# Kernel tuning notes

Hardware: AMD Instinct MI355X
Metric: run time of the kernel (lower is better)

The kernel has to match this reference:

```python
import jax, jax.numpy as jnp
import numpy as np

LL = 1 << 20            # Fastfood padded size (power of 2 >= DD)
DD = 1024 * 768         # out_features * in_features
OUT, IN = 1024, 768


def fwht(v):
    """Unnormalized fast Walsh-Hadamard transform over a length-2^k vector."""
    n = v.shape[0]
    h = 1
    while h < n:
        v = v.reshape(-1, 2, h)
        v = jnp.concatenate([v[:, 0] + v[:, 1], v[:, 0] - v[:, 1]], axis=-1)
        h *= 2
    return v.reshape(n)


def setup_inputs() -> dict:
    key = jax.random.key(0)
    ks = jax.random.split(key, 7)
    x = jax.random.normal(ks[0], (8, 2048, IN), dtype=jnp.float32)
    theta = jax.random.normal(ks[1], (2048,), dtype=jnp.float32)
    W_0 = jax.random.normal(ks[2], (OUT, IN), dtype=jnp.float32) * 0.02
    b = jax.random.normal(ks[3], (OUT,), dtype=jnp.float32) * 0.02
    # Rademacher +/-1 diagonal
    BB = (jax.random.bernoulli(ks[4], 0.5, (LL,)).astype(jnp.float32) * 2.0 - 1.0)
    GG = jax.random.normal(ks[5], (LL,), dtype=jnp.float32)
    Pi = jax.random.permutation(ks[6], LL).astype(jnp.int64)
    return {"x": x, "theta": theta, "W_0": W_0, "b": b, "BB": BB, "GG": GG, "Pi": Pi}


def reference(x, theta, W_0, b, BB, GG, Pi):
    # pad intrinsic parameter to LL (theta.numel() < LL branch)
    theta_pad = jnp.zeros((LL,), dtype=theta.dtype).at[: theta.shape[0]].set(theta)
    # Fastfood: H B theta -> permute -> G diag -> H
    v = fwht(BB * theta_pad)
    v = v[Pi] * GG
    v = fwht(v)
    divisor = jnp.sqrt(LL * jnp.sum(GG * GG))
    update_vec = v[:DD] / (divisor * np.sqrt(float(DD) / LL))
    W_eff = W_0 + update_vec.reshape(OUT, IN)
    return jnp.einsum("bsi,oi->bso", x, W_eff) + b
```

## Files before the change

kernel.cpp:

```cpp
#include <hip/hip_runtime.h>
#include <hip/hip_bf16.h>


#define LL (1 << 20)
#define DD (1024 * 768)
#define OUTF 1024
#define INF 768
#define MROWS 16384

typedef __attribute__((ext_vector_type(8))) short s16x8;
typedef __attribute__((ext_vector_type(4))) float f32x4;

__device__ __forceinline__ unsigned short f2bf(float f) {
    union { float f; unsigned u; } v; v.f = f;
    unsigned r = v.u + 0x7FFF + ((v.u >> 16) & 1);
    return (unsigned short)(r >> 16);
}

__global__ void k3_gather_fwht_lo(const int* __restrict__ Pi, const float* __restrict__ GG,
                                  const float* __restrict__ BB, const float* __restrict__ theta,
                                  float* __restrict__ T, float* __restrict__ partial) {
    __shared__ float s[1024];
    __shared__ float r01s[2048];
    __shared__ float ws4[4];
    const int tid = threadIdx.x;
    const int row = blockIdx.x;
    const int4   pv = ((const int4*)Pi)[row * 256 + tid];
    const float4 gv = ((const float4*)GG)[row * 256 + tid];
    for (int j = tid; j < 2048; j += 256) r01s[j] = BB[j] * theta[j];
    for (int h = 1; h < 1024; h <<= 1) {
        __syncthreads();
        for (int w = tid; w < 1024; w += 256) {
            int rr = w >> 9;
            int b  = w & 511;
            int bh = b & (h - 1);
            int i  = ((b - bh) << 1) + bh + rr * 1024;
            float a = r01s[i], c = r01s[i + h];
            r01s[i] = a + c; r01s[i + h] = a - c;
        }
    }
    float g2 = gv.x * gv.x + gv.y * gv.y + gv.z * gv.z + gv.w * gv.w;
    #pragma unroll
    for (int o = 32; o > 0; o >>= 1) g2 += __shfl_down(g2, o, 64);
    if ((tid & 63) == 0) ws4[tid >> 6] = g2;
    __syncthreads();
    {
        int p; float g, v;
        p = pv.x; g = gv.x;
        v = (r01s[p & 1023] + (((p >> 10) & 1) ? -1.0f : 1.0f) * r01s[1024 + (p & 1023)]) * g;
        s[tid * 4 + 0] = v;
        p = pv.y; g = gv.y;
        v = (r01s[p & 1023] + (((p >> 10) & 1) ? -1.0f : 1.0f) * r01s[1024 + (p & 1023)]) * g;
        s[tid * 4 + 1] = v;
        p = pv.z; g = gv.z;
        v = (r01s[p & 1023] + (((p >> 10) & 1) ? -1.0f : 1.0f) * r01s[1024 + (p & 1023)]) * g;
        s[tid * 4 + 2] = v;
        p = pv.w; g = gv.w;
        v = (r01s[p & 1023] + (((p >> 10) & 1) ? -1.0f : 1.0f) * r01s[1024 + (p & 1023)]) * g;
        s[tid * 4 + 3] = v;
    }
    for (int h = 1; h < 1024; h <<= 1) {
        __syncthreads();
        for (int w = tid; w < 512; w += 256) {
            int bh = w & (h - 1);
            int i  = ((w - bh) << 1) + bh;
            float a = s[i], c = s[i + h];
            s[i] = a + c; s[i + h] = a - c;
        }
    }
    __syncthreads();
    float4 v;
    v.x = s[tid * 4 + 0]; v.y = s[tid * 4 + 1]; v.z = s[tid * 4 + 2]; v.w = s[tid * 4 + 3];
    ((float4*)T)[row * 256 + tid] = v;
    if (tid == 0) partial[row] = ws4[0] + ws4[1] + ws4[2] + ws4[3];
}

__global__ void k4_fwht_hi(float* __restrict__ T, const float* __restrict__ partial,
                           float* __restrict__ S) {
    __shared__ float s[8 * 1025];
    __shared__ float rw[4];
    const int tid = threadIdx.x;
    if (blockIdx.x == 0) {
        float p = partial[tid] + partial[tid + 256] + partial[tid + 512] + partial[tid + 768];
        #pragma unroll
        for (int o = 32; o > 0; o >>= 1) p += __shfl_down(p, o, 64);
        if ((tid & 63) == 0) rw[tid >> 6] = p;
        __syncthreads();
        if (tid == 0) *S = rw[0] + rw[1] + rw[2] + rw[3];
    }
    const int lo0 = blockIdx.x * 8;
    float4* T4 = (float4*)T;
    const int hio = tid >> 1;
    const int q   = tid & 1;
    for (int hb = 0; hb < 8; hb++) {
        int hi = hb * 128 + hio;
        float4 v = T4[hi * 256 + (lo0 >> 2) + q];
        s[(4 * q + 0) * 1025 + hi] = v.x;
        s[(4 * q + 1) * 1025 + hi] = v.y;
        s[(4 * q + 2) * 1025 + hi] = v.z;
        s[(4 * q + 3) * 1025 + hi] = v.w;
    }
    for (int h = 1; h < 1024; h <<= 1) {
        __syncthreads();
        for (int w = tid; w < 8 * 512; w += 256) {
            int col = w >> 9;
            int b   = w & 511;
            int bh  = b & (h - 1);
            int i   = ((b - bh) << 1) + bh;
            float* p = s + col * 1025;
            float a = p[i], c = p[i + h];
            p[i] = a + c; p[i + h] = a - c;
        }
    }
    __syncthreads();
    for (int hb = 0; hb < 8; hb++) {
        int hi = hb * 128 + hio;
        float4 v;
        v.x = s[(4 * q + 0) * 1025 + hi];
        v.y = s[(4 * q + 1) * 1025 + hi];
        v.z = s[(4 * q + 2) * 1025 + hi];
        v.w = s[(4 * q + 3) * 1025 + hi];
        T4[hi * 256 + (lo0 >> 2) + q] = v;
    }
}

__global__ void k5_weff(const float* __restrict__ T, const float* __restrict__ W0,
                        const float* __restrict__ S, ushort* __restrict__ WB) {
    const int i = blockIdx.x * 256 + threadIdx.x;
    const float scale = rsqrtf(*S * (float)DD);
    float4 v = ((const float4*)T)[i];
    float4 w = ((const float4*)W0)[i];
    ushort4 o;
    o.x = f2bf(w.x + v.x * scale);
    o.y = f2bf(w.y + v.y * scale);
    o.z = f2bf(w.z + v.z * scale);
    o.w = f2bf(w.w + v.w * scale);
    ((ushort4*)WB)[i] = o;
}

__global__ void k6_xcast(const float* __restrict__ X, ushort* __restrict__ XB) {
    const int i = blockIdx.x * 256 + threadIdx.x;
    float4 v = ((const float4*)X)[i];
    ushort4 o;
    o.x = f2bf(v.x); o.y = f2bf(v.y); o.z = f2bf(v.z); o.w = f2bf(v.w);
    ((ushort4*)XB)[i] = o;
}

#define BM 128
#define BN 128
#define BK 64

__global__ __launch_bounds__(256)
void k7_gemm(const ushort* __restrict__ A, const ushort* __restrict__ B,
             const float* __restrict__ bias, float* __restrict__ C) {
    __shared__ ushort As[BM * BK];
    __shared__ ushort Bs[BN * BK];
    const int tid  = threadIdx.x;
    const int lane = tid & 63;
    const int wave = tid >> 6;
    const int m0 = blockIdx.x * BM;
    const int n0 = blockIdx.y * BN;
    const int wm = (wave & 1) * 64;
    const int wn = (wave >> 1) * 64;

    const int fr_row = lane & 15;
    const int fr_kg  = lane >> 4;

    f32x4 acc[4][4];
    #pragma unroll
    for (int i = 0; i < 4; i++)
        #pragma unroll
        for (int j = 0; j < 4; j++) acc[i][j] = (f32x4)(0.0f);

    for (int kt = 0; kt < INF; kt += BK) {
        #pragma unroll
        for (int i = 0; i < 4; i++) {
            const int s   = i * 256 + tid;
            const int row = s >> 3;
            const int kc  = (s & 7) ^ (row & 7);
            const ushort* ga = A + (size_t)(m0 + row) * INF + kt + kc * 8;
            const ushort* gb = B + (size_t)(n0 + row) * INF + kt + kc * 8;
            __builtin_amdgcn_global_load_lds(
                (const __attribute__((address_space(1))) void*)ga,
                (__attribute__((address_space(3))) void*)&As[i * 2048 + wave * 512], 16, 0, 0);
            __builtin_amdgcn_global_load_lds(
                (const __attribute__((address_space(1))) void*)gb,
                (__attribute__((address_space(3))) void*)&Bs[i * 2048 + wave * 512], 16, 0, 0);
        }
        __syncthreads();

        #pragma unroll
        for (int ks = 0; ks < 2; ks++) {
            const int kc = ks * 4 + fr_kg;
            s16x8 af[4], bf[4];
            #pragma unroll
            for (int mi = 0; mi < 4; mi++) {
                const int r = wm + mi * 16 + fr_row;
                af[mi] = *(const s16x8*)&As[(r * 8 + (kc ^ (r & 7))) * 8];
            }
            #pragma unroll
            for (int ni = 0; ni < 4; ni++) {
                const int r = wn + ni * 16 + fr_row;
                bf[ni] = *(const s16x8*)&Bs[(r * 8 + (kc ^ (r & 7))) * 8];
            }
            #pragma unroll
            for (int mi = 0; mi < 4; mi++)
                #pragma unroll
                for (int ni = 0; ni < 4; ni++)
                    acc[mi][ni] = __builtin_amdgcn_mfma_f32_16x16x32_bf16(
                        af[mi], bf[ni], acc[mi][ni], 0, 0, 0);
        }
        __syncthreads();
    }

    const int crow = (lane >> 4) * 4;
    const int ccol = lane & 15;
    #pragma unroll
    for (int ni = 0; ni < 4; ni++) {
        const int n = n0 + wn + ni * 16 + ccol;
        const float bv = bias[n];
        #pragma unroll
        for (int mi = 0; mi < 4; mi++) {
            const int mbase = m0 + wm + mi * 16 + crow;
            #pragma unroll
            for (int r = 0; r < 4; r++)
                C[(size_t)(mbase + r) * OUTF + n] = acc[mi][ni][r] + bv;
        }
    }
}

extern "C" void kernel_launch(void* const* d_in, const int* in_sizes, int n_in,
                              void* d_out, int out_size, void* d_ws, size_t ws_size,
                              hipStream_t stream) {
    (void)in_sizes; (void)n_in; (void)out_size; (void)ws_size;
    const float* x     = (const float*)d_in[0];
    const float* theta = (const float*)d_in[1];
    const float* W0    = (const float*)d_in[2];
    const float* bias  = (const float*)d_in[3];
    const float* BB    = (const float*)d_in[4];
    const float* GG    = (const float*)d_in[5];
    const int*   Pi    = (const int*)d_in[6];
    float* out = (float*)d_out;

    char* ws = (char*)d_ws;
    ushort* XB   = (ushort*)ws;
    float*  T    = (float*)(ws + 25165824);
    ushort* WB   = (ushort*)(ws + 29360128);
    float*  S    = (float*)(ws + 30932992);
    float*  PART = (float*)(ws + 30933056);

    k3_gather_fwht_lo<<<1024, 256, 0, stream>>>(Pi, GG, BB, theta, T, PART);
    k4_fwht_hi<<<128, 256, 0, stream>>>(T, PART, S);
    k5_weff  <<<DD/1024, 256, 0, stream>>>(T, W0, S, WB);
    k6_xcast <<<(MROWS*INF)/1024, 256, 0, stream>>>(x, XB);
    k7_gemm  <<<dim3(MROWS/BM, OUTF/BN), 256, 0, stream>>>(XB, WB, bias, out);
}
```

Before: 185.5 us.

## Fuse x-cast into gather-FWHT and W_eff build into high FWHT kernel

The fp32-to-bf16 cast of x moves into the first FWHT kernel: each of its 1024 blocks converts a slice of x after finishing its transform. The W_eff combine (W0 plus scaled transform, cast to bf16) moves into the second FWHT kernel's epilogue. The second kernel now writes only the 768 rows that are used instead of all 1024, and every block recomputes the GG-norm reduction itself. This removes two launches and the full T write-back and re-read. In exchange the first kernel does more work per block, and the redundant per-block reduction adds a little cost.

```diff
diff --git a/kernel.cpp b/kernel.cpp
--- a/kernel.cpp
+++ b/kernel.cpp
@@ -19,6 +19,7 @@
 
 __global__ void k3_gather_fwht_lo(const int* __restrict__ Pi, const float* __restrict__ GG,
                                   const float* __restrict__ BB, const float* __restrict__ theta,
+                                  const float* __restrict__ X, ushort* __restrict__ XB,
                                   float* __restrict__ T, float* __restrict__ partial) {
     __shared__ float s[1024];
     __shared__ float r01s[2048];
@@ -73,23 +74,30 @@
     v.x = s[tid * 4 + 0]; v.y = s[tid * 4 + 1]; v.z = s[tid * 4 + 2]; v.w = s[tid * 4 + 3];
     ((float4*)T)[row * 256 + tid] = v;
     if (tid == 0) partial[row] = ws4[0] + ws4[1] + ws4[2] + ws4[3];
-}
-
-__global__ void k4_fwht_hi(float* __restrict__ T, const float* __restrict__ partial,
-                           float* __restrict__ S) {
+
+    const float4* X4 = (const float4*)X + (size_t)row * 3072;
+    ushort4* XB4 = (ushort4*)XB + (size_t)row * 3072;
+    #pragma unroll
+    for (int j = 0; j < 12; j++) {
+        float4 xv = X4[j * 256 + tid];
+        ushort4 o;
+        o.x = f2bf(xv.x); o.y = f2bf(xv.y); o.z = f2bf(xv.z); o.w = f2bf(xv.w);
+        XB4[j * 256 + tid] = o;
+    }
+}
+
+__global__ void k4_fwht_hi(const float* __restrict__ T, const float* __restrict__ partial,
+                           const float* __restrict__ W0, ushort* __restrict__ WB) {
     __shared__ float s[8 * 1025];
-    __shared__ float rw[4];
+    __shared__ float rw[5];
     const int tid = threadIdx.x;
-    if (blockIdx.x == 0) {
-        float p = partial[tid] + partial[tid + 256] + partial[tid + 512] + partial[tid + 768];
-        #pragma unroll
-        for (int o = 32; o > 0; o >>= 1) p += __shfl_down(p, o, 64);
-        if ((tid & 63) == 0) rw[tid >> 6] = p;
-        __syncthreads();
-        if (tid == 0) *S = rw[0] + rw[1] + rw[2] + rw[3];
-    }
+    float p = partial[tid] + partial[tid + 256] + partial[tid + 512] + partial[tid + 768];
+    #pragma unroll
+    for (int o = 32; o > 0; o >>= 1) p += __shfl_down(p, o, 64);
+    if ((tid & 63) == 0) rw[tid >> 6] = p;
+
     const int lo0 = blockIdx.x * 8;
-    float4* T4 = (float4*)T;
+    const float4* T4 = (const float4*)T;
     const int hio = tid >> 1;
     const int q   = tid & 1;
     for (int hb = 0; hb < 8; hb++) {
@@ -100,50 +108,32 @@
         s[(4 * q + 2) * 1025 + hi] = v.z;
         s[(4 * q + 3) * 1025 + hi] = v.w;
     }
+    __syncthreads();
+    if (tid == 0) rw[4] = rw[0] + rw[1] + rw[2] + rw[3];
     for (int h = 1; h < 1024; h <<= 1) {
-        __syncthreads();
         for (int w = tid; w < 8 * 512; w += 256) {
             int col = w >> 9;
             int b   = w & 511;
             int bh  = b & (h - 1);
             int i   = ((b - bh) << 1) + bh;
-            float* p = s + col * 1025;
-            float a = p[i], c = p[i + h];
-            p[i] = a + c; p[i + h] = a - c;
-        }
-    }
-    __syncthreads();
-    for (int hb = 0; hb < 8; hb++) {
+            float* pp = s + col * 1025;
+            float a = pp[i], c = pp[i + h];
+            pp[i] = a + c; pp[i + h] = a - c;
+        }
+        __syncthreads();
+    }
+    const float scale = rsqrtf(rw[4] * (float)DD);
+    for (int hb = 0; hb < 6; hb++) {
         int hi = hb * 128 + hio;
-        float4 v;
-        v.x = s[(4 * q + 0) * 1025 + hi];
-        v.y = s[(4 * q + 1) * 1025 + hi];
-        v.z = s[(4 * q + 2) * 1025 + hi];
-        v.w = s[(4 * q + 3) * 1025 + hi];
-        T4[hi * 256 + (lo0 >> 2) + q] = v;
-    }
-}
-
-__global__ void k5_weff(const float* __restrict__ T, const float* __restrict__ W0,
-                        const float* __restrict__ S, ushort* __restrict__ WB) {
-    const int i = blockIdx.x * 256 + threadIdx.x;
-    const float scale = rsqrtf(*S * (float)DD);
-    float4 v = ((const float4*)T)[i];
-    float4 w = ((const float4*)W0)[i];
-    ushort4 o;
-    o.x = f2bf(w.x + v.x * scale);
-    o.y = f2bf(w.y + v.y * scale);
-    o.z = f2bf(w.z + v.z * scale);
-    o.w = f2bf(w.w + v.w * scale);
-    ((ushort4*)WB)[i] = o;
-}
-
-__global__ void k6_xcast(const float* __restrict__ X, ushort* __restrict__ XB) {
-    const int i = blockIdx.x * 256 + threadIdx.x;
-    float4 v = ((const float4*)X)[i];
-    ushort4 o;
-    o.x = f2bf(v.x); o.y = f2bf(v.y); o.z = f2bf(v.z); o.w = f2bf(v.w);
-    ((ushort4*)XB)[i] = o;
+        int d  = hi * 1024 + lo0 + 4 * q;
+        float4 w = *(const float4*)&W0[d];
+        ushort4 o;
+        o.x = f2bf(w.x + s[(4 * q + 0) * 1025 + hi] * scale);
+        o.y = f2bf(w.y + s[(4 * q + 1) * 1025 + hi] * scale);
+        o.z = f2bf(w.z + s[(4 * q + 2) * 1025 + hi] * scale);
+        o.w = f2bf(w.w + s[(4 * q + 3) * 1025 + hi] * scale);
+        *(ushort4*)&WB[d] = o;
+    }
 }
 
 #define BM 128
@@ -246,12 +236,9 @@
     ushort* XB   = (ushort*)ws;
     float*  T    = (float*)(ws + 25165824);
     ushort* WB   = (ushort*)(ws + 29360128);
-    float*  S    = (float*)(ws + 30932992);
-    float*  PART = (float*)(ws + 30933056);
-
-    k3_gather_fwht_lo<<<1024, 256, 0, stream>>>(Pi, GG, BB, theta, T, PART);
-    k4_fwht_hi<<<128, 256, 0, stream>>>(T, PART, S);
-    k5_weff  <<<DD/1024, 256, 0, stream>>>(T, W0, S, WB);
-    k6_xcast <<<(MROWS*INF)/1024, 256, 0, stream>>>(x, XB);
+    float*  PART = (float*)(ws + 30932992);
+
+    k3_gather_fwht_lo<<<1024, 256, 0, stream>>>(Pi, GG, BB, theta, x, XB, T, PART);
+    k4_fwht_hi<<<128, 256, 0, stream>>>(T, PART, W0, WB);
     k7_gemm  <<<dim3(MROWS/BM, OUTF/BN), 256, 0, stream>>>(XB, WB, bias, out);
 }
```

After: 180.6 us. 2.7% less time.
